# Kernel tuning notes

Hardware: AMD Instinct MI355X
Metric: run time of the kernel (lower is better)

The kernel has to match this reference:

```python
import jax, jax.numpy as jnp
import numpy as np

B = 16        # sequences (decode batch)
L = 1         # decode: one new token per sequence
HID = 4096
NH = 32       # heads (q == kv, MHA per chunk(3))
HD = 128      # head size
BS = 16       # paged-cache block size
MAXB = 64     # max blocks per sequence (max ctx = 1024)
NB = 1024     # total cache blocks
SCALE = 1.0 / float(np.sqrt(HD))
ROT = HD      # rotary dim == head size


def build_rope_cache():
    inv_freq = 1.0 / (10000.0 ** (jnp.arange(0, ROT, 2, dtype=jnp.float32) / ROT))
    t = jnp.arange(2048, dtype=jnp.float32)
    freqs = jnp.einsum('i,j->ij', t, inv_freq)          # [2048, 64]
    return jnp.concatenate([jnp.cos(freqs), jnp.sin(freqs)], axis=-1)  # [2048, 128]


def setup_inputs() -> dict:
    key = jax.random.key(0)
    ks = jax.random.split(key, 8)
    hidden_states = jax.random.normal(ks[0], (B, L, HID), jnp.float32) * 0.02
    qkv_w = jax.random.normal(ks[1], (3 * HID, HID), jnp.float32) * 0.02
    out_w = jax.random.normal(ks[2], (HID, HID), jnp.float32) * 0.02
    cos_sin_cache = build_rope_cache()
    key_cache = jax.random.normal(ks[3], (NB, BS, NH, HD), jnp.float32)
    value_cache = jax.random.normal(ks[4], (NB, BS, NH, HD), jnp.float32)
    context_lengths = jax.random.randint(ks[5], (B,), 1, MAXB * BS + 1, jnp.int32)
    position_ids = (context_lengths - 1).reshape(B, L).astype(jnp.int32)
    # unique blocks per sequence (no scatter collisions)
    block_tables = jax.random.permutation(ks[6], NB)[: B * MAXB].reshape(B, MAXB).astype(jnp.int32)
    last = context_lengths - 1
    slots = (block_tables[jnp.arange(B), last // BS] * BS + last % BS).astype(jnp.int32)
    return {
        'hidden_states': hidden_states, 'qkv_w': qkv_w, 'out_w': out_w,
        'cos_sin_cache': cos_sin_cache, 'key_cache': key_cache, 'value_cache': value_cache,
        'position_ids': position_ids, 'block_tables': block_tables,
        'slots': slots, 'context_lengths': context_lengths,
    }


def _rope_neox(x, cos, sin):
    # x: [T, H, HD]; cos/sin: [T, 1, HD//2]
    x1, x2 = x[..., : ROT // 2], x[..., ROT // 2:]
    return jnp.concatenate([x1 * cos - x2 * sin, x2 * cos + x1 * sin], axis=-1)


def reference(hidden_states, qkv_w, out_w, cos_sin_cache, key_cache, value_cache,
              position_ids, block_tables, slots, context_lengths):
    bsz, max_len, hidden = hidden_states.shape
    T = bsz * max_len
    # fused QKV projection, chunk(3)
    qkv = hidden_states.reshape(T, hidden) @ qkv_w.T           # [T, 3*HID]
    q, k, v = jnp.split(qkv, 3, axis=-1)
    q = q.reshape(T, NH, HD)
    k = k.reshape(T, NH, HD)
    v = v.reshape(T, NH, HD)
    # RoPE (neox style) on q and k
    cs = cos_sin_cache[position_ids.reshape(-1)]               # [T, ROT]
    cos = cs[:, : ROT // 2][:, None, :]
    sin = cs[:, ROT // 2:][:, None, :]
    q = _rope_neox(q, cos, sin)
    k = _rope_neox(k, cos, sin)
    # reshape_and_cache: scatter new k/v into paged cache at `slots`
    kc = key_cache.reshape(NB * BS, NH, HD).at[slots].set(k)
    vc = value_cache.reshape(NB * BS, NH, HD).at[slots].set(v)
    kc = kc.reshape(NB, BS, NH, HD)
    vc = vc.reshape(NB, BS, NH, HD)
    # paged attention: gather each sequence's blocks via block_tables
    S = MAXB * BS
    Kg = kc[block_tables].reshape(bsz, S, NH, HD)              # [B, S, H, D]
    Vg = vc[block_tables].reshape(bsz, S, NH, HD)
    scores = jnp.einsum('bhd,bshd->bhs', q, Kg) * SCALE        # [B, H, S]
    valid = jnp.arange(S, dtype=jnp.int32)[None, None, :] < context_lengths[:, None, None]
    scores = jnp.where(valid, scores, jnp.float32(-1e30))
    p = jax.nn.softmax(scores, axis=-1)
    attn = jnp.einsum('bhs,bshd->bhd', p, Vg).reshape(T, NH * HD)
    return (attn @ out_w.T).reshape(bsz, max_len, hidden)
```

## Files before the change

kernel.cpp:

```cpp
#include <hip/hip_runtime.h>
#include <math.h>

#define NH 32
#define HD 128
#define BS 16
#define MAXB 64
#define HID 4096
#define NBATCH 16
#define QKV_R 12288
#define SCALE 0.08838834764831845f

__global__ __launch_bounds__(256) void gemv16_v2(
    const float* __restrict__ x, const float* __restrict__ W,
    float* __restrict__ y, int R) {
  const int r0 = blockIdx.x * 8;
  const int tid = threadIdx.x;
  const int wave = tid >> 6, lane = tid & 63;
  const int b0 = wave * 4;

  float acc[8][4];
#pragma unroll
  for (int r = 0; r < 8; ++r)
#pragma unroll
    for (int bb = 0; bb < 4; ++bb) acc[r][bb] = 0.f;

#pragma unroll 2
  for (int it = 0; it < 16; ++it) {
    const int j = it * 256 + lane * 4;
    float4 wv[8];
#pragma unroll
    for (int r = 0; r < 8; ++r)
      wv[r] = *reinterpret_cast<const float4*>(&W[(size_t)(r0 + r) * 4096 + j]);
    float4 xv[4];
#pragma unroll
    for (int bb = 0; bb < 4; ++bb)
      xv[bb] = *reinterpret_cast<const float4*>(&x[(size_t)(b0 + bb) * 4096 + j]);
#pragma unroll
    for (int r = 0; r < 8; ++r)
#pragma unroll
      for (int bb = 0; bb < 4; ++bb)
        acc[r][bb] += wv[r].x * xv[bb].x + wv[r].y * xv[bb].y +
                      wv[r].z * xv[bb].z + wv[r].w * xv[bb].w;
  }

#pragma unroll
  for (int r = 0; r < 8; ++r)
#pragma unroll
    for (int bb = 0; bb < 4; ++bb) {
      float v = acc[r][bb];
#pragma unroll
      for (int off = 32; off; off >>= 1) v += __shfl_xor(v, off, 64);
      if (lane == 0) y[(size_t)(b0 + bb) * R + r0 + r] = v;
    }
}

__global__ __launch_bounds__(256) void attn_decode_v2(
    const float* __restrict__ qkv, const float* __restrict__ cs_cache,
    const float* __restrict__ kcache, const float* __restrict__ vcache,
    const int* __restrict__ pos_ids, const int* __restrict__ btab,
    const int* __restrict__ ctx_len, float* __restrict__ attn_out) {
  const int b = blockIdx.x >> 5;
  const int h = blockIdx.x & 31;
  const int tid = threadIdx.x;
  const int wave = tid >> 6, lane = tid & 63;
  const int grp = lane >> 3, sub = lane & 7;
  const int gid = wave * 8 + grp;

  __shared__ float q_rot[HD], k_rot[HD], v_new[HD];
  __shared__ float scores[MAXB * BS];
  __shared__ int blk_base[MAXB];
  __shared__ float redm[4], reds[4];
  __shared__ float ow[4][HD];

  const int ctx = ctx_len[b];
  const int last = ctx - 1;
  const int pos = pos_ids[b];
  const float* qp = qkv + (size_t)b * QKV_R + h * HD;
  const float* kp = qp + 4096;
  const float* vp = qp + 8192;
  const float* cs = cs_cache + (size_t)pos * HD;

  if (tid < 64) {
    const float c = cs[tid], s = cs[64 + tid];
    const float a1 = qp[tid], a2 = qp[tid + 64];
    q_rot[tid] = a1 * c - a2 * s;
    q_rot[tid + 64] = a2 * c + a1 * s;
    const float b1 = kp[tid], b2 = kp[tid + 64];
    k_rot[tid] = b1 * c - b2 * s;
    k_rot[tid + 64] = b2 * c + b1 * s;
  } else if (tid < 192) {
    v_new[tid - 64] = vp[tid - 64];
  } else {
    blk_base[tid - 192] = btab[b * MAXB + (tid - 192)];
  }
  __syncthreads();

  float4 qf[4];
#pragma unroll
  for (int i = 0; i < 4; ++i)
    qf[i] = *reinterpret_cast<const float4*>(&q_rot[sub * 4 + i * 32]);

#pragma unroll 2
  for (int t = gid; t < ctx; t += 32) {
    float4 kv[4];
    if (t == last) {
#pragma unroll
      for (int i = 0; i < 4; ++i)
        kv[i] = *reinterpret_cast<const float4*>(&k_rot[sub * 4 + i * 32]);
    } else {
      const int blk = blk_base[t >> 4];
      const float* kr = kcache + ((((size_t)blk << 4) + (t & 15)) * NH + h) * HD;
#pragma unroll
      for (int i = 0; i < 4; ++i)
        kv[i] = *reinterpret_cast<const float4*>(&kr[sub * 4 + i * 32]);
    }
    float d0 = kv[0].x * qf[0].x + kv[0].y * qf[0].y + kv[0].z * qf[0].z + kv[0].w * qf[0].w;
    float d1 = kv[1].x * qf[1].x + kv[1].y * qf[1].y + kv[1].z * qf[1].z + kv[1].w * qf[1].w;
    float d2 = kv[2].x * qf[2].x + kv[2].y * qf[2].y + kv[2].z * qf[2].z + kv[2].w * qf[2].w;
    float d3 = kv[3].x * qf[3].x + kv[3].y * qf[3].y + kv[3].z * qf[3].z + kv[3].w * qf[3].w;
    float d = (d0 + d1) + (d2 + d3);
    d += __shfl_xor(d, 1, 64);
    d += __shfl_xor(d, 2, 64);
    d += __shfl_xor(d, 4, 64);
    if (sub == 0) scores[t] = d * SCALE;
  }
  __syncthreads();

  float m = -1e30f;
  for (int s = tid; s < ctx; s += 256) m = fmaxf(m, scores[s]);
#pragma unroll
  for (int off = 32; off; off >>= 1) m = fmaxf(m, __shfl_xor(m, off, 64));
  if (lane == 0) redm[wave] = m;
  __syncthreads();
  m = fmaxf(fmaxf(redm[0], redm[1]), fmaxf(redm[2], redm[3]));

  float ssum = 0.f;
  for (int s = tid; s < ctx; s += 256) {
    const float e = expf(scores[s] - m);
    scores[s] = e;
    ssum += e;
  }
#pragma unroll
  for (int off = 32; off; off >>= 1) ssum += __shfl_xor(ssum, off, 64);
  if (lane == 0) reds[wave] = ssum;
  __syncthreads();
  const float inv_sum = 1.f / (reds[0] + reds[1] + reds[2] + reds[3]);

  float4 oacc[4];
#pragma unroll
  for (int i = 0; i < 4; ++i) oacc[i] = make_float4(0.f, 0.f, 0.f, 0.f);

#pragma unroll 2
  for (int t = gid; t < ctx; t += 32) {
    const float p = scores[t];
    float4 vv[4];
    if (t == last) {
#pragma unroll
      for (int i = 0; i < 4; ++i)
        vv[i] = *reinterpret_cast<const float4*>(&v_new[sub * 4 + i * 32]);
    } else {
      const int blk = blk_base[t >> 4];
      const float* vr = vcache + ((((size_t)blk << 4) + (t & 15)) * NH + h) * HD;
#pragma unroll
      for (int i = 0; i < 4; ++i)
        vv[i] = *reinterpret_cast<const float4*>(&vr[sub * 4 + i * 32]);
    }
#pragma unroll
    for (int i = 0; i < 4; ++i) {
      oacc[i].x += p * vv[i].x;
      oacc[i].y += p * vv[i].y;
      oacc[i].z += p * vv[i].z;
      oacc[i].w += p * vv[i].w;
    }
  }

#pragma unroll
  for (int i = 0; i < 4; ++i) {
#pragma unroll
    for (int off = 8; off <= 32; off <<= 1) {
      oacc[i].x += __shfl_xor(oacc[i].x, off, 64);
      oacc[i].y += __shfl_xor(oacc[i].y, off, 64);
      oacc[i].z += __shfl_xor(oacc[i].z, off, 64);
      oacc[i].w += __shfl_xor(oacc[i].w, off, 64);
    }
  }
  if (grp == 0) {
#pragma unroll
    for (int i = 0; i < 4; ++i)
      *reinterpret_cast<float4*>(&ow[wave][sub * 4 + i * 32]) = oacc[i];
  }
  __syncthreads();
  if (tid < HD) {
    const float o = (ow[0][tid] + ow[1][tid] + ow[2][tid] + ow[3][tid]) * inv_sum;
    attn_out[(size_t)b * HID + h * HD + tid] = o;
  }
}

extern "C" void kernel_launch(void* const* d_in, const int* in_sizes, int n_in,
                              void* d_out, int out_size, void* d_ws, size_t ws_size,
                              hipStream_t stream) {
  const float* hidden = (const float*)d_in[0];
  const float* qkv_w  = (const float*)d_in[1];
  const float* out_w  = (const float*)d_in[2];
  const float* cs     = (const float*)d_in[3];
  const float* kc     = (const float*)d_in[4];
  const float* vc     = (const float*)d_in[5];
  const int* pos      = (const int*)d_in[6];
  const int* bt       = (const int*)d_in[7];
  const int* cl       = (const int*)d_in[9];
  float* out = (float*)d_out;

  float* ws_qkv  = (float*)d_ws;
  float* ws_attn = ws_qkv + NBATCH * QKV_R;

  gemv16_v2<<<QKV_R / 8, 256, 0, stream>>>(hidden, qkv_w, ws_qkv, QKV_R);
  attn_decode_v2<<<NBATCH * NH, 256, 0, stream>>>(ws_qkv, cs, kc, vc, pos, bt, cl, ws_attn);
  gemv16_v2<<<HID / 8, 256, 0, stream>>>(ws_attn, out_w, out, HID);
}
```

Baseline: 161.3 us.

## Split decode attention across context chunks with a separate combine kernel

Replaces the one-block-per-(batch,head) attention kernel with a split-KV (flash-decoding) scheme. Each of 8 chunks of 128 tokens gets its own block, which writes partial output, max and sum to workspace, and a new combine kernel merges them with log-sum-exp rescaling. This raises grid parallelism from 512 blocks and evens out load across sequences of very different context lengths, at the cost of an extra kernel launch and a partial-result round trip through global memory.

Result: slower. 165.0 us (+2.3%).

```diff
diff --git a/kernel.cpp b/kernel.cpp
--- a/kernel.cpp
+++ b/kernel.cpp
@@ -9,6 +9,8 @@
 #define NBATCH 16
 #define QKV_R 12288
 #define SCALE 0.08838834764831845f
+#define TPC 128
+#define NCHUNK 8
 
 __global__ __launch_bounds__(256) void gemv16_v2(
     const float* __restrict__ x, const float* __restrict__ W,
@@ -54,26 +56,33 @@
     }
 }
 
-__global__ __launch_bounds__(256) void attn_decode_v2(
+__global__ __launch_bounds__(256) void attn_split(
     const float* __restrict__ qkv, const float* __restrict__ cs_cache,
     const float* __restrict__ kcache, const float* __restrict__ vcache,
     const int* __restrict__ pos_ids, const int* __restrict__ btab,
-    const int* __restrict__ ctx_len, float* __restrict__ attn_out) {
-  const int b = blockIdx.x >> 5;
-  const int h = blockIdx.x & 31;
+    const int* __restrict__ ctx_len, float* __restrict__ o_part,
+    float* __restrict__ m_part, float* __restrict__ l_part) {
+  const int bh = blockIdx.x;
+  const int b = bh >> 5, h = bh & 31;
+  const int c = blockIdx.y;
+  const int ctx = ctx_len[b];
+  const int t0 = c * TPC;
+  if (t0 >= ctx) return;
+  const int tend = min(t0 + TPC, ctx);
+  const int n = tend - t0;
+  const int last = ctx - 1;
+
   const int tid = threadIdx.x;
   const int wave = tid >> 6, lane = tid & 63;
   const int grp = lane >> 3, sub = lane & 7;
   const int gid = wave * 8 + grp;
 
   __shared__ float q_rot[HD], k_rot[HD], v_new[HD];
-  __shared__ float scores[MAXB * BS];
-  __shared__ int blk_base[MAXB];
+  __shared__ float scores[TPC];
+  __shared__ int blk_base[TPC / BS];
   __shared__ float redm[4], reds[4];
   __shared__ float ow[4][HD];
 
-  const int ctx = ctx_len[b];
-  const int last = ctx - 1;
   const int pos = pos_ids[b];
   const float* qp = qkv + (size_t)b * QKV_R + h * HD;
   const float* kp = qp + 4096;
@@ -81,17 +90,19 @@
   const float* cs = cs_cache + (size_t)pos * HD;
 
   if (tid < 64) {
-    const float c = cs[tid], s = cs[64 + tid];
+    const float co = cs[tid], si = cs[64 + tid];
     const float a1 = qp[tid], a2 = qp[tid + 64];
-    q_rot[tid] = a1 * c - a2 * s;
-    q_rot[tid + 64] = a2 * c + a1 * s;
+    q_rot[tid] = a1 * co - a2 * si;
+    q_rot[tid + 64] = a2 * co + a1 * si;
     const float b1 = kp[tid], b2 = kp[tid + 64];
-    k_rot[tid] = b1 * c - b2 * s;
-    k_rot[tid + 64] = b2 * c + b1 * s;
+    k_rot[tid] = b1 * co - b2 * si;
+    k_rot[tid + 64] = b2 * co + b1 * si;
   } else if (tid < 192) {
     v_new[tid - 64] = vp[tid - 64];
-  } else {
-    blk_base[tid - 192] = btab[b * MAXB + (tid - 192)];
+  } else if (tid < 192 + TPC / BS) {
+    const int i = tid - 192;
+    const int bt_idx = (t0 >> 4) + i;
+    blk_base[i] = (bt_idx < MAXB) ? btab[b * MAXB + bt_idx] : 0;
   }
   __syncthreads();
 
@@ -100,15 +111,14 @@
   for (int i = 0; i < 4; ++i)
     qf[i] = *reinterpret_cast<const float4*>(&q_rot[sub * 4 + i * 32]);
 
-#pragma unroll 2
-  for (int t = gid; t < ctx; t += 32) {
+  for (int t = t0 + gid; t < tend; t += 32) {
     float4 kv[4];
     if (t == last) {
 #pragma unroll
       for (int i = 0; i < 4; ++i)
         kv[i] = *reinterpret_cast<const float4*>(&k_rot[sub * 4 + i * 32]);
     } else {
-      const int blk = blk_base[t >> 4];
+      const int blk = blk_base[(t - t0) >> 4];
       const float* kr = kcache + ((((size_t)blk << 4) + (t & 15)) * NH + h) * HD;
 #pragma unroll
       for (int i = 0; i < 4; ++i)
@@ -122,12 +132,11 @@
     d += __shfl_xor(d, 1, 64);
     d += __shfl_xor(d, 2, 64);
     d += __shfl_xor(d, 4, 64);
-    if (sub == 0) scores[t] = d * SCALE;
-  }
-  __syncthreads();
-
-  float m = -1e30f;
-  for (int s = tid; s < ctx; s += 256) m = fmaxf(m, scores[s]);
+    if (sub == 0) scores[t - t0] = d * SCALE;
+  }
+  __syncthreads();
+
+  float m = (tid < n) ? scores[tid] : -1e30f;
 #pragma unroll
   for (int off = 32; off; off >>= 1) m = fmaxf(m, __shfl_xor(m, off, 64));
   if (lane == 0) redm[wave] = m;
@@ -135,31 +144,30 @@
   m = fmaxf(fmaxf(redm[0], redm[1]), fmaxf(redm[2], redm[3]));
 
   float ssum = 0.f;
-  for (int s = tid; s < ctx; s += 256) {
-    const float e = expf(scores[s] - m);
-    scores[s] = e;
-    ssum += e;
+  if (tid < n) {
+    const float e = expf(scores[tid] - m);
+    scores[tid] = e;
+    ssum = e;
   }
 #pragma unroll
   for (int off = 32; off; off >>= 1) ssum += __shfl_xor(ssum, off, 64);
   if (lane == 0) reds[wave] = ssum;
   __syncthreads();
-  const float inv_sum = 1.f / (reds[0] + reds[1] + reds[2] + reds[3]);
+  const float l = reds[0] + reds[1] + reds[2] + reds[3];
 
   float4 oacc[4];
 #pragma unroll
   for (int i = 0; i < 4; ++i) oacc[i] = make_float4(0.f, 0.f, 0.f, 0.f);
 
-#pragma unroll 2
-  for (int t = gid; t < ctx; t += 32) {
-    const float p = scores[t];
+  for (int t = t0 + gid; t < tend; t += 32) {
+    const float p = scores[t - t0];
     float4 vv[4];
     if (t == last) {
 #pragma unroll
       for (int i = 0; i < 4; ++i)
         vv[i] = *reinterpret_cast<const float4*>(&v_new[sub * 4 + i * 32]);
     } else {
-      const int blk = blk_base[t >> 4];
+      const int blk = blk_base[(t - t0) >> 4];
       const float* vr = vcache + ((((size_t)blk << 4) + (t & 15)) * NH + h) * HD;
 #pragma unroll
       for (int i = 0; i < 4; ++i)
@@ -191,9 +199,34 @@
   }
   __syncthreads();
   if (tid < HD) {
-    const float o = (ow[0][tid] + ow[1][tid] + ow[2][tid] + ow[3][tid]) * inv_sum;
-    attn_out[(size_t)b * HID + h * HD + tid] = o;
-  }
+    const float o = ow[0][tid] + ow[1][tid] + ow[2][tid] + ow[3][tid];
+    o_part[((size_t)bh * NCHUNK + c) * HD + tid] = o;
+    if (tid == 0) {
+      m_part[bh * NCHUNK + c] = m;
+      l_part[bh * NCHUNK + c] = l;
+    }
+  }
+}
+
+__global__ __launch_bounds__(128) void attn_combine(
+    const float* __restrict__ o_part, const float* __restrict__ m_part,
+    const float* __restrict__ l_part, const int* __restrict__ ctx_len,
+    float* __restrict__ attn_out) {
+  const int bh = blockIdx.x;
+  const int b = bh >> 5, h = bh & 31;
+  const int ctx = ctx_len[b];
+  const int nc = (ctx + TPC - 1) / TPC;
+  const int d = threadIdx.x;
+
+  float M = -1e30f;
+  for (int c = 0; c < nc; ++c) M = fmaxf(M, m_part[bh * NCHUNK + c]);
+  float L = 0.f, o = 0.f;
+  for (int c = 0; c < nc; ++c) {
+    const float sc = expf(m_part[bh * NCHUNK + c] - M);
+    L += l_part[bh * NCHUNK + c] * sc;
+    o += o_part[((size_t)bh * NCHUNK + c) * HD + d] * sc;
+  }
+  attn_out[(size_t)b * HID + h * HD + d] = o / L;
 }
 
 extern "C" void kernel_launch(void* const* d_in, const int* in_sizes, int n_in,
@@ -212,8 +245,13 @@
 
   float* ws_qkv  = (float*)d_ws;
   float* ws_attn = ws_qkv + NBATCH * QKV_R;
+  float* ws_op   = ws_attn + NBATCH * HID;
+  float* ws_m    = ws_op + (size_t)NBATCH * NH * NCHUNK * HD;
+  float* ws_l    = ws_m + NBATCH * NH * NCHUNK;
 
   gemv16_v2<<<QKV_R / 8, 256, 0, stream>>>(hidden, qkv_w, ws_qkv, QKV_R);
-  attn_decode_v2<<<NBATCH * NH, 256, 0, stream>>>(ws_qkv, cs, kc, vc, pos, bt, cl, ws_attn);
+  attn_split<<<dim3(NBATCH * NH, NCHUNK), 256, 0, stream>>>(
+      ws_qkv, cs, kc, vc, pos, bt, cl, ws_op, ws_m, ws_l);
+  attn_combine<<<NBATCH * NH, 128, 0, stream>>>(ws_op, ws_m, ws_l, cl, ws_attn);
   gemv16_v2<<<HID / 8, 256, 0, stream>>>(ws_attn, out_w, out, HID);
 }
```
